# Kernel optimization log

Measured on AMD Instinct MI355X. Metric: run time of the kernel, lower is better.

Reference implementation:

```python
import jax, jax.numpy as jnp
import numpy as np

B, T, C, H = 4, 2048, 1024, 16
D = C // H  # head dim = 64


def setup_inputs() -> dict:
    key = jax.random.key(0)
    ks = jax.random.split(key, 8)
    s = 1.0 / np.sqrt(C)
    return {
        "x": jax.random.normal(ks[0], (B, T, C), jnp.float32),
        "mask": jax.random.randint(ks[1], (B, T), 0, 2, jnp.int32),
        "Wq": jax.random.normal(ks[2], (C, C), jnp.float32) * s,
        "bq": jnp.zeros((C,), jnp.float32),
        "Wk": jax.random.normal(ks[3], (C, C), jnp.float32) * s,
        "bk": jnp.zeros((C,), jnp.float32),
        "Wv": jax.random.normal(ks[4], (C, C), jnp.float32) * s,
        "bv": jnp.zeros((C,), jnp.float32),
    }


def reference(x, mask, Wq, bq, Wk, bk, Wv, bv):
    # QKV projections (nn.Linear: x @ W.T + b); W stored here as [out,in] -> use W.T
    q = x @ Wq.T + bq
    k = x @ Wk.T + bk
    v = x @ Wv.T + bv
    # split heads: [B,T,C] -> [B,H,T,D]
    q = q.reshape(B, T, H, D).transpose(0, 2, 1, 3)
    k = k.reshape(B, T, H, D).transpose(0, 2, 1, 3)
    v = v.reshape(B, T, H, D).transpose(0, 2, 1, 3)
    # scaled dot-product attention scores [B,H,T,T]
    attn = jnp.einsum("bhqd,bhkd->bhqk", q, k) / jnp.sqrt(jnp.float32(D))
    # additive mask over key positions: attn - inf*(1-mask), expressed stably
    big_neg = jnp.float32(-1e30)
    attn = jnp.where(mask[:, None, None, :] > 0, attn, big_neg)
    attn = jax.nn.softmax(attn, axis=-1)
    # dropout p=0 -> identity
    y = jnp.einsum("bhqk,bhkd->bhqd", attn, v)
    # merge heads: [B,H,T,D] -> [B,T,C]
    return y.transpose(0, 2, 1, 3).reshape(B, T, C)
```

## Files before the change

### kernel.cpp

```cpp
#include <hip/hip_runtime.h>
#include <stdint.h>

#define BB 4
#define TT 2048
#define CC 1024
#define HH 16
#define DD 64
#define MM (BB * TT)

typedef unsigned short u16;
typedef unsigned int   u32;
typedef __attribute__((ext_vector_type(8))) short short8;
typedef _Float16 half8  __attribute__((ext_vector_type(8)));
typedef __fp16   fp16x2 __attribute__((ext_vector_type(2)));
typedef __attribute__((ext_vector_type(4))) float f32x4;
typedef __attribute__((ext_vector_type(4))) unsigned short u16x4;
typedef __attribute__((ext_vector_type(4))) unsigned int u32x4;

#if __has_builtin(__builtin_amdgcn_exp2f)
#define EXP2(x) __builtin_amdgcn_exp2f(x)
#else
#define EXP2(x) __expf(0.69314718055994531f * (x))
#endif

__device__ inline u16 f2bf(float f) {
    union { float f; unsigned u; } v; v.f = f;
    unsigned r = 0x7fffu + ((v.u >> 16) & 1u);
    return (u16)((v.u + r) >> 16);
}
__device__ inline u16 f2h(float f) {
    union { _Float16 h; u16 u; } c; c.h = (_Float16)f; return c.u;
}
__device__ inline u32 pkh(float a, float b) {
    union { fp16x2 h; u32 u; } c;
    c.h = __builtin_amdgcn_cvt_pkrtz(a, b);
    return c.u;
}
__device__ inline void load_lds16(const u16* g, u16* l) {
    __builtin_amdgcn_global_load_lds((const __attribute__((address_space(1))) void*)g,
                                     (__attribute__((address_space(3))) void*)l, 16, 0, 0);
}

#define NX (MM * CC / 4)
#define NW (CC * CC / 4)
__global__ void cvt_all(const float* __restrict__ x,  const float* __restrict__ Wq,
                        const float* __restrict__ Wk, const float* __restrict__ Wv,
                        u16* __restrict__ xb, u16* __restrict__ Wb) {
    int i = blockIdx.x * blockDim.x + threadIdx.x;
    const float* src; u16* dst; int j;
    if (i < NX)               { src = x;  dst = xb;                       j = i; }
    else if (i < NX + NW)     { src = Wq; dst = Wb;                       j = i - NX; }
    else if (i < NX + 2 * NW) { src = Wk; dst = Wb + (size_t)CC * CC;     j = i - NX - NW; }
    else if (i < NX + 3 * NW) { src = Wv; dst = Wb + (size_t)2 * CC * CC; j = i - NX - 2 * NW; }
    else return;
    float4 v = ((const float4*)src)[j];
    u16x4 o;
    o.x = f2bf(v.x); o.y = f2bf(v.y); o.z = f2bf(v.z); o.w = f2bf(v.w);
    ((u16x4*)dst)[j] = o;
}

__global__ void qkv_gemm(const u16* __restrict__ xb, const u16* __restrict__ Wb,
                         const float* __restrict__ bq, const float* __restrict__ bk,
                         const float* __restrict__ bv,
                         u16* __restrict__ Qh, u16* __restrict__ Kh, u16* __restrict__ Vt)
{
    const int z = blockIdx.z;
    const u16* W = Wb + (size_t)z * CC * CC;
    const float* bias = (z == 0) ? bq : ((z == 1) ? bk : bv);
    const float scale = (z == 0) ? 0.18033688011112042f : 1.0f;

    __shared__ __align__(16) u16 As[128][32];
    __shared__ __align__(16) u16 Bs[128][32];

    const int tid = threadIdx.x;
    const int l  = tid & 63, w = tid >> 6;
    const int wm = w >> 1,  wn = w & 1;
    const int lr = l & 15,  lq = l >> 4;
    const int m0 = blockIdx.y * 128, n0 = blockIdx.x * 128;

    f32x4 acc[4][4] = {};

    const u16* aLDS = (z == 2) ? &As[0][0] : &Bs[0][0];
    const u16* bLDS = (z == 2) ? &Bs[0][0] : &As[0][0];

    for (int kt = 0; kt < CC; kt += 32) {
        __syncthreads();
        #pragma unroll
        for (int r = 0; r < 2; ++r) {
            int c   = (r * 4 + w) * 64 + l;
            int row = c >> 2, kc = c & 3;
            const u16* ga = xb + (size_t)(m0 + row) * CC + kt + kc * 8;
            load_lds16(ga, &As[0][0] + (size_t)c * 8);
            const u16* gb = W + (size_t)(n0 + row) * CC + kt + kc * 8;
            load_lds16(gb, &Bs[0][0] + (size_t)c * 8);
        }
        __syncthreads();

        short8 af[4], bfr[4];
        #pragma unroll
        for (int mi = 0; mi < 4; ++mi)
            af[mi] = *(const short8*)(aLDS + (size_t)(wm * 64 + mi * 16 + lr) * 32 + lq * 8);
        #pragma unroll
        for (int ni = 0; ni < 4; ++ni)
            bfr[ni] = *(const short8*)(bLDS + (size_t)(wn * 64 + ni * 16 + lr) * 32 + lq * 8);
        #pragma unroll
        for (int mi = 0; mi < 4; ++mi)
            #pragma unroll
            for (int ni = 0; ni < 4; ++ni)
                acc[mi][ni] = __builtin_amdgcn_mfma_f32_16x16x32_bf16(
                    af[mi], bfr[ni], acc[mi][ni], 0, 0, 0);
    }

    if (z == 2) {
        #pragma unroll
        for (int ni = 0; ni < 4; ++ni) {
            int n = n0 + wn * 64 + ni * 16 + lr;
            float bvv = bias[n];
            int h = n >> 6, d = n & 63;
            #pragma unroll
            for (int mi = 0; mi < 4; ++mi) {
                int mbase = m0 + wm * 64 + mi * 16 + lq * 4;
                int b = mbase >> 11, t0 = mbase & (TT - 1);
                int tg = t0 & ~31;
                int s0 = (((t0 >> 2) & 3) << 3) + (((t0 >> 4) & 1) << 2);
                u16x4 pkv;
                #pragma unroll
                for (int r = 0; r < 4; ++r)
                    pkv[r] = f2h(acc[mi][ni][r] + bvv);
                *(u16x4*)&Vt[((size_t)(b * HH + h) * DD + d) * TT + tg + s0] = pkv;
            }
        }
    } else {
        u16* out = (z == 0) ? Qh : Kh;
        #pragma unroll
        for (int mi = 0; mi < 4; ++mi) {
            int nb = n0 + wm * 64 + mi * 16 + lq * 4;
            float4 b4 = *(const float4*)&bias[nb];
            int h = nb >> 6, d0 = nb & 63;
            #pragma unroll
            for (int ni = 0; ni < 4; ++ni) {
                int m = m0 + wn * 64 + ni * 16 + lr;
                int b = m >> 11, t = m & (TT - 1);
                u16x4 pkv;
                pkv.x = f2h((acc[mi][ni][0] + b4.x) * scale);
                pkv.y = f2h((acc[mi][ni][1] + b4.y) * scale);
                pkv.z = f2h((acc[mi][ni][2] + b4.z) * scale);
                pkv.w = f2h((acc[mi][ni][3] + b4.w) * scale);
                *(u16x4*)&out[((size_t)(b * HH + h) * TT + t) * DD + d0] = pkv;
            }
        }
    }
}

__global__ __launch_bounds__(256, 2)
void attn_kernel(const u16* __restrict__ Qh, const u16* __restrict__ Kh,
                 const u16* __restrict__ Vt, const int* __restrict__ mask,
                 float* __restrict__ out)
{
    const int qt = blockIdx.x;
    const int h  = blockIdx.y;
    const int b  = blockIdx.z;
    const int tid = threadIdx.x;
    const int l  = tid & 63, w = tid >> 6;
    const int lr = l & 15,  lq = l >> 4;

    __shared__ __align__(16) u16 KsL[2][32 * 64];
    __shared__ __align__(16) u16 VsL[2][64 * 32];

    const size_t base = (size_t)(b * HH + h) * TT * DD;
    const int q0 = qt * 256 + w * 64;

    half8 qf[4][2];
    #pragma unroll
    for (int qg = 0; qg < 4; ++qg)
        #pragma unroll
        for (int c = 0; c < 2; ++c)
            qf[qg][c] = *(const half8*)(Qh + base + (size_t)(q0 + qg * 16 + lr) * DD
                                        + c * 32 + lq * 8);

    const int kkey = tid >> 3, kqx = tid & 7;
    const int kq = kqx ^ (kkey & 7);
    const u16* kgp = Kh + base + (size_t)kkey * DD + kq * 8;
    u16* kl0 = &KsL[0][0] + tid * 8;
    const int vdd = tid >> 2, vqx = tid & 3;
    const int vq = vqx ^ ((vdd >> 1) & 3);
    const u16* vgp = Vt + base + (size_t)vdd * TT + vq * 8;
    u16* vl0 = &VsL[0][0] + tid * 8;

    const int* mbase_p = mask + b * TT + 4 * lq;

    u32x4 onesbits = { 0x3C003C00u, 0x3C003C00u, 0x3C003C00u, 0x3C003C00u };
    half8 ones = (half8&)onesbits;

    f32x4 o[4][5] = {};

    const int NT = TT / 32;

    load_lds16(kgp, kl0);
    load_lds16(vgp, vl0);
    __syncthreads();

    for (int kt = 0; kt < NT; ++kt) {
        const int p = kt & 1;
        if (kt + 1 < NT) {
            load_lds16(kgp + (size_t)(kt + 1) * 32 * DD, kl0 + (p ^ 1) * (32 * 64));
            load_lds16(vgp + (size_t)(kt + 1) * 32,      vl0 + (p ^ 1) * (64 * 32));
        }
        int4 ma = *(const int4*)(mbase_p + kt * 32);
        int4 mb = *(const int4*)(mbase_p + kt * 32 + 16);

        half8 kf[2][2];
        #pragma unroll
        for (int kg = 0; kg < 2; ++kg) {
            int key = kg * 16 + lr;
            #pragma unroll
            for (int c = 0; c < 2; ++c)
                kf[kg][c] = *(const half8*)&KsL[p][key * 64
                                + (((c * 4 + lq) ^ (key & 7)) * 8)];
        }

        f32x4 s[2][4];
        #pragma unroll
        for (int kg = 0; kg < 2; ++kg)
            #pragma unroll
            for (int qg = 0; qg < 4; ++qg) {
                f32x4 zz = {};
                zz = __builtin_amdgcn_mfma_f32_16x16x32_f16(kf[kg][0], qf[qg][0], zz, 0, 0, 0);
                zz = __builtin_amdgcn_mfma_f32_16x16x32_f16(kf[kg][1], qf[qg][1], zz, 0, 0, 0);
                s[kg][qg] = zz;
            }

        float f00 = (float)ma.x, f01 = (float)ma.y, f02 = (float)ma.z, f03 = (float)ma.w;
        float f10 = (float)mb.x, f11 = (float)mb.y, f12 = (float)mb.z, f13 = (float)mb.w;
        half8 pf[4];
        #pragma unroll
        for (int qg = 0; qg < 4; ++qg) {
            u32x4 pk;
            pk[0] = pkh(EXP2(s[0][qg][0]) * f00, EXP2(s[0][qg][1]) * f01);
            pk[1] = pkh(EXP2(s[0][qg][2]) * f02, EXP2(s[0][qg][3]) * f03);
            pk[2] = pkh(EXP2(s[1][qg][0]) * f10, EXP2(s[1][qg][1]) * f11);
            pk[3] = pkh(EXP2(s[1][qg][2]) * f12, EXP2(s[1][qg][3]) * f13);
            pf[qg] = (half8&)pk;
        }

        #pragma unroll
        for (int dg = 0; dg < 4; ++dg) {
            int d = dg * 16 + lr;
            half8 vf = *(const half8*)&VsL[p][d * 32 + ((lq ^ ((d >> 1) & 3)) * 8)];
            #pragma unroll
            for (int qg = 0; qg < 4; ++qg)
                o[qg][dg] = __builtin_amdgcn_mfma_f32_16x16x32_f16(pf[qg], vf, o[qg][dg], 0, 0, 0);
        }
        #pragma unroll
        for (int qg = 0; qg < 4; ++qg)
            o[qg][4] = __builtin_amdgcn_mfma_f32_16x16x32_f16(pf[qg], ones, o[qg][4], 0, 0, 0);

        __syncthreads();
    }

    #pragma unroll
    for (int qg = 0; qg < 4; ++qg)
        #pragma unroll
        for (int r = 0; r < 4; ++r) {
            float inv = 1.f / o[qg][4][r];
            int t = q0 + qg * 16 + lq * 4 + r;
            float* op = out + (size_t)(b * TT + t) * CC + h * DD;
            #pragma unroll
            for (int dg = 0; dg < 4; ++dg)
                op[dg * 16 + lr] = o[qg][dg][r] * inv;
        }
}

extern "C" void kernel_launch(void* const* d_in, const int* in_sizes, int n_in,
                              void* d_out, int out_size, void* d_ws, size_t ws_size,
                              hipStream_t stream) {
    const float* x    = (const float*)d_in[0];
    const int*   mask = (const int*)d_in[1];
    const float* Wq   = (const float*)d_in[2];
    const float* bq   = (const float*)d_in[3];
    const float* Wk   = (const float*)d_in[4];
    const float* bk   = (const float*)d_in[5];
    const float* Wv   = (const float*)d_in[6];
    const float* bv   = (const float*)d_in[7];
    float* out = (float*)d_out;

    u16* xb = (u16*)d_ws;
    u16* Wb = xb + (size_t)MM * CC;
    u16* Qh = Wb + (size_t)3 * CC * CC;
    u16* Kh = Qh + (size_t)MM * CC;
    u16* Vt = Kh + (size_t)MM * CC;

    {
        int total = NX + 3 * NW;
        cvt_all<<<(total + 255) / 256, 256, 0, stream>>>(x, Wq, Wk, Wv, xb, Wb);
    }

    qkv_gemm<<<dim3(CC / 128, MM / 128, 3), 256, 0, stream>>>(xb, Wb, bq, bk, bv, Qh, Kh, Vt);

    attn_kernel<<<dim3(TT / 256, HH, BB), 256, 0, stream>>>(Qh, Kh, Vt, mask, out);
}
```

Measured before the change: 256.2 us.

## Double K-tile depth in GEMM and attention, precompute float mask, reorder grid

The QKV GEMM now stages 64-wide K tiles with an XOR-swizzled LDS layout, which halves the number of barriers and targets bank conflicts. The attention kernel processes 64 keys per iteration in two 32-key halves and double-buffers larger K/V tiles, again halving barrier count. The int mask is converted to float once in the conversion kernel so attention skips the per-tile int-to-float conversion. The grid is reordered with heads along x. The cost is more LDS and more registers, which could reduce occupancy.

```diff
diff --git a/kernel.cpp b/kernel.cpp
--- a/kernel.cpp
+++ b/kernel.cpp
@@ -43,16 +43,26 @@
 
 #define NX (MM * CC / 4)
 #define NW (CC * CC / 4)
+#define NM (BB * TT / 4)
 __global__ void cvt_all(const float* __restrict__ x,  const float* __restrict__ Wq,
                         const float* __restrict__ Wk, const float* __restrict__ Wv,
-                        u16* __restrict__ xb, u16* __restrict__ Wb) {
+                        const int* __restrict__ mask,
+                        u16* __restrict__ xb, u16* __restrict__ Wb, float* __restrict__ fm) {
     int i = blockIdx.x * blockDim.x + threadIdx.x;
+    if (i >= NX + 3 * NW) {
+        int j = i - (NX + 3 * NW);
+        if (j < NM) {
+            int4 mm = ((const int4*)mask)[j];
+            float4 o = { (float)mm.x, (float)mm.y, (float)mm.z, (float)mm.w };
+            ((float4*)fm)[j] = o;
+        }
+        return;
+    }
     const float* src; u16* dst; int j;
     if (i < NX)               { src = x;  dst = xb;                       j = i; }
     else if (i < NX + NW)     { src = Wq; dst = Wb;                       j = i - NX; }
     else if (i < NX + 2 * NW) { src = Wk; dst = Wb + (size_t)CC * CC;     j = i - NX - NW; }
-    else if (i < NX + 3 * NW) { src = Wv; dst = Wb + (size_t)2 * CC * CC; j = i - NX - 2 * NW; }
-    else return;
+    else                      { src = Wv; dst = Wb + (size_t)2 * CC * CC; j = i - NX - 2 * NW; }
     float4 v = ((const float4*)src)[j];
     u16x4 o;
     o.x = f2bf(v.x); o.y = f2bf(v.y); o.z = f2bf(v.z); o.w = f2bf(v.w);
@@ -69,8 +79,8 @@
     const float* bias = (z == 0) ? bq : ((z == 1) ? bk : bv);
     const float scale = (z == 0) ? 0.18033688011112042f : 1.0f;
 
-    __shared__ __align__(16) u16 As[128][32];
-    __shared__ __align__(16) u16 Bs[128][32];
+    __shared__ __align__(16) u16 As[128 * 64];
+    __shared__ __align__(16) u16 Bs[128 * 64];
 
     const int tid = threadIdx.x;
     const int l  = tid & 63, w = tid >> 6;
@@ -80,35 +90,43 @@
 
     f32x4 acc[4][4] = {};
 
-    const u16* aLDS = (z == 2) ? &As[0][0] : &Bs[0][0];
-    const u16* bLDS = (z == 2) ? &Bs[0][0] : &As[0][0];
-
-    for (int kt = 0; kt < CC; kt += 32) {
+    const u16* aLDS = (z == 2) ? As : Bs;
+    const u16* bLDS = (z == 2) ? Bs : As;
+
+    for (int kt = 0; kt < CC; kt += 64) {
         __syncthreads();
         #pragma unroll
-        for (int r = 0; r < 2; ++r) {
-            int c   = (r * 4 + w) * 64 + l;
-            int row = c >> 2, kc = c & 3;
-            const u16* ga = xb + (size_t)(m0 + row) * CC + kt + kc * 8;
-            load_lds16(ga, &As[0][0] + (size_t)c * 8);
-            const u16* gb = W + (size_t)(n0 + row) * CC + kt + kc * 8;
-            load_lds16(gb, &Bs[0][0] + (size_t)c * 8);
+        for (int r = 0; r < 4; ++r) {
+            int c   = r * 256 + tid;
+            int row = c >> 3, q = c & 7;
+            int kc  = q ^ (row & 7);
+            load_lds16(xb + (size_t)(m0 + row) * CC + kt + kc * 8, As + (size_t)c * 8);
+            load_lds16(W  + (size_t)(n0 + row) * CC + kt + kc * 8, Bs + (size_t)c * 8);
         }
         __syncthreads();
 
-        short8 af[4], bfr[4];
-        #pragma unroll
-        for (int mi = 0; mi < 4; ++mi)
-            af[mi] = *(const short8*)(aLDS + (size_t)(wm * 64 + mi * 16 + lr) * 32 + lq * 8);
-        #pragma unroll
-        for (int ni = 0; ni < 4; ++ni)
-            bfr[ni] = *(const short8*)(bLDS + (size_t)(wn * 64 + ni * 16 + lr) * 32 + lq * 8);
-        #pragma unroll
-        for (int mi = 0; mi < 4; ++mi)
-            #pragma unroll
-            for (int ni = 0; ni < 4; ++ni)
-                acc[mi][ni] = __builtin_amdgcn_mfma_f32_16x16x32_bf16(
-                    af[mi], bfr[ni], acc[mi][ni], 0, 0, 0);
+        #pragma unroll
+        for (int s = 0; s < 2; ++s) {
+            short8 af[4], bfr[4];
+            #pragma unroll
+            for (int mi = 0; mi < 4; ++mi) {
+                int row = wm * 64 + mi * 16 + lr;
+                af[mi] = *(const short8*)(aLDS + (size_t)row * 64
+                                          + (((s * 4 + lq) ^ (row & 7)) * 8));
+            }
+            #pragma unroll
+            for (int ni = 0; ni < 4; ++ni) {
+                int row = wn * 64 + ni * 16 + lr;
+                bfr[ni] = *(const short8*)(bLDS + (size_t)row * 64
+                                           + (((s * 4 + lq) ^ (row & 7)) * 8));
+            }
+            #pragma unroll
+            for (int mi = 0; mi < 4; ++mi)
+                #pragma unroll
+                for (int ni = 0; ni < 4; ++ni)
+                    acc[mi][ni] = __builtin_amdgcn_mfma_f32_16x16x32_bf16(
+                        af[mi], bfr[ni], acc[mi][ni], 0, 0, 0);
+        }
     }
 
     if (z == 2) {
@@ -154,18 +172,18 @@
 
 __global__ __launch_bounds__(256, 2)
 void attn_kernel(const u16* __restrict__ Qh, const u16* __restrict__ Kh,
-                 const u16* __restrict__ Vt, const int* __restrict__ mask,
+                 const u16* __restrict__ Vt, const float* __restrict__ fm,
                  float* __restrict__ out)
 {
-    const int qt = blockIdx.x;
-    const int h  = blockIdx.y;
+    const int h  = blockIdx.x;
+    const int qt = blockIdx.y;
     const int b  = blockIdx.z;
     const int tid = threadIdx.x;
     const int l  = tid & 63, w = tid >> 6;
     const int lr = l & 15,  lq = l >> 4;
 
-    __shared__ __align__(16) u16 KsL[2][32 * 64];
-    __shared__ __align__(16) u16 VsL[2][64 * 32];
+    __shared__ __align__(16) u16 KsL[2][4096];
+    __shared__ __align__(16) u16 VsL[2][4096];
 
     const size_t base = (size_t)(b * HH + h) * TT * DD;
     const int q0 = qt * 256 + w * 64;
@@ -181,79 +199,90 @@
     const int kkey = tid >> 3, kqx = tid & 7;
     const int kq = kqx ^ (kkey & 7);
     const u16* kgp = Kh + base + (size_t)kkey * DD + kq * 8;
-    u16* kl0 = &KsL[0][0] + tid * 8;
+    u16* kl = &KsL[0][0] + tid * 8;
     const int vdd = tid >> 2, vqx = tid & 3;
     const int vq = vqx ^ ((vdd >> 1) & 3);
     const u16* vgp = Vt + base + (size_t)vdd * TT + vq * 8;
-    u16* vl0 = &VsL[0][0] + tid * 8;
-
-    const int* mbase_p = mask + b * TT + 4 * lq;
+    u16* vl = &VsL[0][0] + tid * 8;
+
+    const float* fmp = fm + b * TT + 4 * lq;
 
     u32x4 onesbits = { 0x3C003C00u, 0x3C003C00u, 0x3C003C00u, 0x3C003C00u };
     half8 ones = (half8&)onesbits;
 
     f32x4 o[4][5] = {};
 
-    const int NT = TT / 32;
-
-    load_lds16(kgp, kl0);
-    load_lds16(vgp, vl0);
+    const int NT = TT / 64;
+
+    load_lds16(kgp,            kl);
+    load_lds16(kgp + 32 * DD,  kl + 2048);
+    load_lds16(vgp,            vl);
+    load_lds16(vgp + 32,       vl + 2048);
     __syncthreads();
 
     for (int kt = 0; kt < NT; ++kt) {
         const int p = kt & 1;
         if (kt + 1 < NT) {
-            load_lds16(kgp + (size_t)(kt + 1) * 32 * DD, kl0 + (p ^ 1) * (32 * 64));
-            load_lds16(vgp + (size_t)(kt + 1) * 32,      vl0 + (p ^ 1) * (64 * 32));
-        }
-        int4 ma = *(const int4*)(mbase_p + kt * 32);
-        int4 mb = *(const int4*)(mbase_p + kt * 32 + 16);
-
-        half8 kf[2][2];
-        #pragma unroll
-        for (int kg = 0; kg < 2; ++kg) {
-            int key = kg * 16 + lr;
-            #pragma unroll
-            for (int c = 0; c < 2; ++c)
-                kf[kg][c] = *(const half8*)&KsL[p][key * 64
-                                + (((c * 4 + lq) ^ (key & 7)) * 8)];
-        }
-
-        f32x4 s[2][4];
-        #pragma unroll
-        for (int kg = 0; kg < 2; ++kg)
+            const u16* kg2 = kgp + (size_t)(kt + 1) * 64 * DD;
+            const u16* vg2 = vgp + (kt + 1) * 64;
+            load_lds16(kg2,           kl + (p ^ 1) * 4096);
+            load_lds16(kg2 + 32 * DD, kl + (p ^ 1) * 4096 + 2048);
+            load_lds16(vg2,           vl + (p ^ 1) * 4096);
+            load_lds16(vg2 + 32,      vl + (p ^ 1) * 4096 + 2048);
+        }
+        const u16* Kp = &KsL[0][0] + p * 4096;
+        const u16* Vp = &VsL[0][0] + p * 4096;
+
+        half8 pf[4][2];
+        #pragma unroll
+        for (int sub = 0; sub < 2; ++sub) {
+            half8 kf0[2], kf1[2];
+            #pragma unroll
+            for (int c = 0; c < 2; ++c) {
+                int sw = ((c * 4 + lq) ^ (lr & 7)) * 8;
+                kf0[c] = *(const half8*)(Kp + sub * 2048 + (size_t)lr * 64 + sw);
+                kf1[c] = *(const half8*)(Kp + sub * 2048 + (size_t)(16 + lr) * 64 + sw);
+            }
+            f32x4 s0[4], s1[4];
             #pragma unroll
             for (int qg = 0; qg < 4; ++qg) {
-                f32x4 zz = {};
-                zz = __builtin_amdgcn_mfma_f32_16x16x32_f16(kf[kg][0], qf[qg][0], zz, 0, 0, 0);
-                zz = __builtin_amdgcn_mfma_f32_16x16x32_f16(kf[kg][1], qf[qg][1], zz, 0, 0, 0);
-                s[kg][qg] = zz;
-            }
-
-        float f00 = (float)ma.x, f01 = (float)ma.y, f02 = (float)ma.z, f03 = (float)ma.w;
-        float f10 = (float)mb.x, f11 = (float)mb.y, f12 = (float)mb.z, f13 = (float)mb.w;
-        half8 pf[4];
-        #pragma unroll
-        for (int qg = 0; qg < 4; ++qg) {
-            u32x4 pk;
-            pk[0] = pkh(EXP2(s[0][qg][0]) * f00, EXP2(s[0][qg][1]) * f01);
-            pk[1] = pkh(EXP2(s[0][qg][2]) * f02, EXP2(s[0][qg][3]) * f03);
-            pk[2] = pkh(EXP2(s[1][qg][0]) * f10, EXP2(s[1][qg][1]) * f11);
-            pk[3] = pkh(EXP2(s[1][qg][2]) * f12, EXP2(s[1][qg][3]) * f13);
-            pf[qg] = (half8&)pk;
+                f32x4 z0 = {}, z1 = {};
+                z0 = __builtin_amdgcn_mfma_f32_16x16x32_f16(kf0[0], qf[qg][0], z0, 0, 0, 0);
+                z0 = __builtin_amdgcn_mfma_f32_16x16x32_f16(kf0[1], qf[qg][1], z0, 0, 0, 0);
+                z1 = __builtin_amdgcn_mfma_f32_16x16x32_f16(kf1[0], qf[qg][0], z1, 0, 0, 0);
+                z1 = __builtin_amdgcn_mfma_f32_16x16x32_f16(kf1[1], qf[qg][1], z1, 0, 0, 0);
+                s0[qg] = z0; s1[qg] = z1;
+            }
+            float4 fa = *(const float4*)(fmp + kt * 64 + sub * 32);
+            float4 fb = *(const float4*)(fmp + kt * 64 + sub * 32 + 16);
+            #pragma unroll
+            for (int qg = 0; qg < 4; ++qg) {
+                u32x4 pk;
+                pk[0] = pkh(EXP2(s0[qg][0]) * fa.x, EXP2(s0[qg][1]) * fa.y);
+                pk[1] = pkh(EXP2(s0[qg][2]) * fa.z, EXP2(s0[qg][3]) * fa.w);
+                pk[2] = pkh(EXP2(s1[qg][0]) * fb.x, EXP2(s1[qg][1]) * fb.y);
+                pk[3] = pkh(EXP2(s1[qg][2]) * fb.z, EXP2(s1[qg][3]) * fb.w);
+                pf[qg][sub] = (half8&)pk;
+            }
         }
 
         #pragma unroll
         for (int dg = 0; dg < 4; ++dg) {
             int d = dg * 16 + lr;
-            half8 vf = *(const half8*)&VsL[p][d * 32 + ((lq ^ ((d >> 1) & 3)) * 8)];
-            #pragma unroll
-            for (int qg = 0; qg < 4; ++qg)
-                o[qg][dg] = __builtin_amdgcn_mfma_f32_16x16x32_f16(pf[qg], vf, o[qg][dg], 0, 0, 0);
-        }
-        #pragma unroll
-        for (int qg = 0; qg < 4; ++qg)
-            o[qg][4] = __builtin_amdgcn_mfma_f32_16x16x32_f16(pf[qg], ones, o[qg][4], 0, 0, 0);
+            int sw = ((lq ^ ((d >> 1) & 3)) * 8);
+            half8 vf0 = *(const half8*)(Vp + (size_t)d * 32 + sw);
+            half8 vf1 = *(const half8*)(Vp + 2048 + (size_t)d * 32 + sw);
+            #pragma unroll
+            for (int qg = 0; qg < 4; ++qg) {
+                o[qg][dg] = __builtin_amdgcn_mfma_f32_16x16x32_f16(pf[qg][0], vf0, o[qg][dg], 0, 0, 0);
+                o[qg][dg] = __builtin_amdgcn_mfma_f32_16x16x32_f16(pf[qg][1], vf1, o[qg][dg], 0, 0, 0);
+            }
+        }
+        #pragma unroll
+        for (int qg = 0; qg < 4; ++qg) {
+            o[qg][4] = __builtin_amdgcn_mfma_f32_16x16x32_f16(pf[qg][0], ones, o[qg][4], 0, 0, 0);
+            o[qg][4] = __builtin_amdgcn_mfma_f32_16x16x32_f16(pf[qg][1], ones, o[qg][4], 0, 0, 0);
+        }
 
         __syncthreads();
     }
@@ -289,13 +318,14 @@
     u16* Qh = Wb + (size_t)3 * CC * CC;
     u16* Kh = Qh + (size_t)MM * CC;
     u16* Vt = Kh + (size_t)MM * CC;
+    float* fm = (float*)(Vt + (size_t)MM * CC);
 
     {
-        int total = NX + 3 * NW;
-        cvt_all<<<(total + 255) / 256, 256, 0, stream>>>(x, Wq, Wk, Wv, xb, Wb);
+        int total = NX + 3 * NW + NM;
+        cvt_all<<<(total + 255) / 256, 256, 0, stream>>>(x, Wq, Wk, Wv, mask, xb, Wb, fm);
     }
 
     qkv_gemm<<<dim3(CC / 128, MM / 128, 3), 256, 0, stream>>>(xb, Wb, bq, bk, bv, Qh, Kh, Vt);
 
-    attn_kernel<<<dim3(TT / 256, HH, BB), 256, 0, stream>>>(Qh, Kh, Vt, mask, out);
-}
+    attn_kernel<<<dim3(HH, TT / 256, BB), 256, 0, stream>>>(Qh, Kh, Vt, fm, out);
+}
```

New measurement: 253.4 us. No clear change (-1.1%).
